# Performance work log

Measured on AMD Instinct MI355X. Metric: run time of the kernel, lower is better.

The kernel has to match this reference:

```python
import jax, jax.numpy as jnp
import numpy as np

N = 50000      # n_nodes
E = 800000     # n_edges (avg degree 16)
IN, HID, CLS = 128, 128, 40


def setup_inputs() -> dict:
    key = jax.random.key(0)
    ks = jax.random.split(key, 9)
    features = jax.random.normal(ks[0], (N, IN), dtype=jnp.float32)
    src = jax.random.randint(ks[1], (E,), 0, N)
    dst = jax.random.randint(ks[2], (E,), 0, N)
    # GraphConv weights (glorot-ish scale) and biases
    W0 = jax.random.normal(ks[3], (IN, HID), dtype=jnp.float32) / np.sqrt(IN).astype(np.float32)
    b0 = jnp.zeros((HID,), jnp.float32)
    W1 = jax.random.normal(ks[4], (HID, HID), dtype=jnp.float32) / np.sqrt(HID).astype(np.float32)
    b1 = jnp.zeros((HID,), jnp.float32)
    W2 = jax.random.normal(ks[5], (HID, CLS), dtype=jnp.float32) / np.sqrt(HID).astype(np.float32)
    b2 = jnp.zeros((CLS,), jnp.float32)
    return {"features": features, "src": src, "dst": dst,
            "W0": W0, "b0": b0, "W1": W1, "b1": b1, "W2": W2, "b2": b2}


def _degree_norms(src, dst, dtype):
    # DGL GraphConv norm='both': D_out^{-1/2} on source side, D_in^{-1/2} on dest side,
    # degrees clamped to a minimum of 1.
    ones = jnp.ones(src.shape[0], dtype)
    deg_out = jax.ops.segment_sum(ones, src, num_segments=N)
    deg_in = jax.ops.segment_sum(ones, dst, num_segments=N)
    norm_out = jnp.where(deg_out > 0, deg_out, 1.0) ** -0.5
    norm_in = jnp.where(deg_in > 0, deg_in, 1.0) ** -0.5
    return norm_out, norm_in


def _graph_conv(h, src, dst, norm_out, norm_in, W, b, act):
    # h' = D_in^{-1/2} A D_out^{-1/2} h W + b ; optional relu
    h = (h * norm_out[:, None]) @ W            # dense transform first (in >= out)
    agg = jax.ops.segment_sum(h[src], dst, num_segments=N)  # sparse aggregation
    out = agg * norm_in[:, None] + b
    return jax.nn.relu(out) if act else out


def reference(features, src, dst, W0, b0, W1, b1, W2, b2):
    norm_out, norm_in = _degree_norms(src, dst, features.dtype)
    # dropout is identity in eval mode
    h = _graph_conv(features, src, dst, norm_out, norm_in, W0, b0, True)
    h = _graph_conv(h, src, dst, norm_out, norm_in, W1, b1, True)
    h = _graph_conv(h, src, dst, norm_out, norm_in, W2, b2, False)
    return h
```

## Files before the change

kernel.cpp:

```cpp
#include <hip/hip_runtime.h>
#include <hip/hip_fp16.h>


static constexpr int NN  = 50000;
static constexpr int NE  = 800000;
static constexpr int HID = 128;
static constexpr int CLS = 40;
static constexpr int CAP = 48;

static constexpr int NGEMM  = (NN + 127) / 128;
static constexpr int NBUILD = (NE + 1023) / 1024;
static constexpr int NPREP  = 8;

typedef __attribute__((ext_vector_type(8))) _Float16 f16x8;
typedef __attribute__((ext_vector_type(4))) float    f32x4;

__device__ __forceinline__ void gemm128_body(const float* __restrict__ X,
                                             const float* __restrict__ W,
                                             __half* __restrict__ Y,
                                             int tileIdx, float* As, float* Bs) {
    constexpr int BSTR = 132;
    const int tid = threadIdx.x;
    const int rowBase = tileIdx * 128;

    const int bkk = tid >> 3;
    const int bc4 = tid & 7;
    const float* wrow = W + (size_t)bkk * 128 + bc4 * 16;

    const int rt = tid & 15;
    const int ct = tid >> 4;

    float acc[8][8];
    #pragma unroll
    for (int j = 0; j < 8; ++j)
        #pragma unroll
        for (int i = 0; i < 8; ++i) acc[j][i] = 0.f;

    float4 xv[4], wv[4];

    auto loadA = [&](int s) {
        #pragma unroll
        for (int i = 0; i < 4; ++i) {
            int f = tid + 256 * i;
            int r = f >> 3;
            int kc = f & 7;
            int grow = rowBase + r;
            xv[i] = (grow < NN)
                ? *(const float4*)(X + (size_t)grow * 128 + s * 32 + kc * 4)
                : make_float4(0.f, 0.f, 0.f, 0.f);
        }
    };
    auto loadB = [&](int s) {
        const float* p = wrow + (size_t)s * 32 * 128;
        #pragma unroll
        for (int i = 0; i < 4; ++i) wv[i] = ((const float4*)p)[i];
    };
    auto writeLDS = [&]() {
        #pragma unroll
        for (int i = 0; i < 4; ++i) {
            int f = tid + 256 * i;
            int r = f >> 3;
            int kc = f & 7;
            int pc = ((r >> 2) + kc) & 31;
            int base = pc * 4 + (r & 3);
            const float* v = (const float*)&xv[i];
            #pragma unroll
            for (int c = 0; c < 4; ++c)
                As[(kc * 4 + c) * 128 + base] = v[c];
        }
        #pragma unroll
        for (int i = 0; i < 4; ++i)
            *(float4*)&Bs[bkk * BSTR + bc4 * 16 + i * 4] = wv[i];
    };

    loadA(0); loadB(0);
    for (int s = 0; s < 4; ++s) {
        writeLDS();
        __syncthreads();
        if (s < 3) { loadA(s + 1); loadB(s + 1); }
        #pragma unroll 8
        for (int k = 0; k < 32; ++k) {
            int kc = k >> 2;
            int pa0 = (rt + kc) & 31;
            int pa1 = (rt + 16 + kc) & 31;
            float4 a0 = *(const float4*)&As[k * 128 + pa0 * 4];
            float4 a1 = *(const float4*)&As[k * 128 + pa1 * 4];
            float4 b0 = *(const float4*)&Bs[k * BSTR + ct * 8];
            float4 b1 = *(const float4*)&Bs[k * BSTR + ct * 8 + 4];
            float a[8] = {a0.x, a0.y, a0.z, a0.w, a1.x, a1.y, a1.z, a1.w};
            float b[8] = {b0.x, b0.y, b0.z, b0.w, b1.x, b1.y, b1.z, b1.w};
            #pragma unroll
            for (int j = 0; j < 8; ++j)
                #pragma unroll
                for (int ii = 0; ii < 8; ++ii)
                    acc[j][ii] = fmaf(a[j], b[ii], acc[j][ii]);
        }
        __syncthreads();
    }
    union Pack { __half2 h2[4]; uint4 u; };
    #pragma unroll
    for (int j = 0; j < 8; ++j) {
        int row = rowBase + ((j < 4) ? (4 * rt + j) : (64 + 4 * rt + (j - 4)));
        if (row < NN) {
            Pack p;
            #pragma unroll
            for (int q = 0; q < 4; ++q)
                p.h2[q] = __halves2half2(__float2half_rn(acc[j][2 * q]),
                                         __float2half_rn(acc[j][2 * q + 1]));
            *(uint4*)(Y + (size_t)row * 128 + ct * 8) = p.u;
        }
    }
}

__global__ __launch_bounds__(256) void fused_kernel(const float* __restrict__ X,
                                                    const float* __restrict__ W0,
                                                    __half* __restrict__ Y,
                                                    const int* __restrict__ src,
                                                    const int* __restrict__ dst,
                                                    int* __restrict__ deg_out,
                                                    int* __restrict__ cnt,
                                                    unsigned short* __restrict__ colbkt,
                                                    const float* __restrict__ W1,
                                                    __half* __restrict__ W1t) {
    __shared__ float As[32 * 128];
    __shared__ float Bs[32 * 132];
    int b = blockIdx.x;
    if (b < NGEMM) {
        gemm128_body(X, W0, Y, b, As, Bs);
    } else if (b < NGEMM + NBUILD) {
        int base = (b - NGEMM) * 1024 + threadIdx.x;
        int e[4], s[4], d[4];
        #pragma unroll
        for (int i = 0; i < 4; ++i) {
            e[i] = base + 256 * i;
            int ec = e[i] < NE ? e[i] : NE - 1;
            s[i] = src[ec];
            d[i] = dst[ec];
        }
        #pragma unroll
        for (int i = 0; i < 4; ++i)
            if (e[i] < NE) atomicAdd(&deg_out[s[i]], 1);
        int slot[4];
        #pragma unroll
        for (int i = 0; i < 4; ++i)
            slot[i] = (e[i] < NE) ? atomicAdd(&cnt[d[i]], 1) : CAP;
        #pragma unroll
        for (int i = 0; i < 4; ++i)
            if (slot[i] < CAP)
                colbkt[(size_t)d[i] * CAP + slot[i]] = (unsigned short)s[i];
    } else {
        int gid = (b - NGEMM - NBUILD) * 256 + threadIdx.x;
        int n = gid >> 4, q = gid & 15;
        union { __half h[8]; uint4 u; } p;
        #pragma unroll
        for (int j = 0; j < 8; ++j)
            p.h[j] = __float2half_rn(W1[(size_t)(q * 8 + j) * 128 + n]);
        ((uint4*)W1t)[n * 16 + ((q + n) & 15)] = p.u;
    }
}

__global__ __launch_bounds__(256) void gemm1_mfma(const __half* __restrict__ H,
                                                  const __half* __restrict__ W1t,
                                                  const float* __restrict__ norm_out,
                                                  __half* __restrict__ T) {
    __shared__ __half Ws[128 * 128];
    const int tid = threadIdx.x;
    #pragma unroll
    for (int i = 0; i < 8; ++i)
        ((uint4*)Ws)[tid + 256 * i] = ((const uint4*)W1t)[tid + 256 * i];

    const int wv   = tid >> 6;
    const int lane = tid & 63;
    const int m    = lane & 15;
    const int quad = lane >> 4;
    const int rowW = blockIdx.x * 64 + wv * 16;

    union AB { uint4 u; f16x8 h; };
    AB a[4];
    int arow = rowW + m;
    if (arow >= NN) arow = NN - 1;
    const uint4* hp = (const uint4*)(H + (size_t)arow * 128);
    #pragma unroll
    for (int kc = 0; kc < 4; ++kc)
        a[kc].u = hp[kc * 4 + quad];

    __syncthreads();

    f32x4 acc[8];
    #pragma unroll
    for (int nt = 0; nt < 8; ++nt) acc[nt] = (f32x4){0.f, 0.f, 0.f, 0.f};

    #pragma unroll
    for (int kc = 0; kc < 4; ++kc) {
        #pragma unroll
        for (int nt = 0; nt < 8; ++nt) {
            int n = nt * 16 + m;
            int q = kc * 4 + quad;
            AB bf;
            bf.u = ((const uint4*)Ws)[n * 16 + ((q + n) & 15)];
            acc[nt] = __builtin_amdgcn_mfma_f32_16x16x32_f16(a[kc].h, bf.h, acc[nt], 0, 0, 0);
        }
    }

    float nmv[4];
    #pragma unroll
    for (int r = 0; r < 4; ++r) {
        int row = rowW + quad * 4 + r;
        nmv[r] = (row < NN) ? norm_out[row] : 0.f;
    }
    #pragma unroll
    for (int nt = 0; nt < 8; ++nt) {
        int coln = nt * 16 + m;
        #pragma unroll
        for (int r = 0; r < 4; ++r) {
            int row = rowW + quad * 4 + r;
            if (row < NN)
                T[(size_t)row * 128 + coln] = __float2half_rn(acc[nt][r] * nmv[r]);
        }
    }
}

__global__ __launch_bounds__(256) void gemm40_kernel(const __half* __restrict__ X,
                                                     const float* __restrict__ W,
                                                     const float* __restrict__ norm_out,
                                                     __half* __restrict__ Y) {
    __shared__ float As[32 * 128];
    __shared__ float Bs[32 * 40];
    const int tid = threadIdx.x;
    const int rowBase = blockIdx.x * 128;

    const int rt = tid & 31;
    const int ct = tid >> 5;

    float acc[4][5];
    #pragma unroll
    for (int j = 0; j < 4; ++j)
        #pragma unroll
        for (int c = 0; c < 5; ++c) acc[j][c] = 0.f;

    uint4 xu[2];
    float4 wv[2];

    auto loadA = [&](int s) {
        #pragma unroll
        for (int i = 0; i < 2; ++i) {
            int f = tid + 256 * i;
            int r = f >> 2;
            int c = f & 3;
            int grow = rowBase + r;
            xu[i] = (grow < NN)
                ? *(const uint4*)(X + (size_t)grow * 128 + s * 32 + c * 8)
                : make_uint4(0, 0, 0, 0);
        }
    };
    auto loadB = [&](int s) {
        #pragma unroll
        for (int i = 0; i < 2; ++i) {
            int f = tid + 256 * i;
            if (f < 320) {
                int kk = f / 10, c4 = f - kk * 10;
                wv[i] = *(const float4*)(W + (size_t)(s * 32 + kk) * 40 + c4 * 4);
            }
        }
    };
    auto writeLDS = [&]() {
        #pragma unroll
        for (int i = 0; i < 2; ++i) {
            int f = tid + 256 * i;
            int r = f >> 2;
            int c = f & 3;
            const __half2* hp = (const __half2*)&xu[i];
            #pragma unroll
            for (int q = 0; q < 4; ++q) {
                float2 f2 = __half22float2(hp[q]);
                int k0 = c * 8 + 2 * q;
                int pc = ((r >> 2) + (k0 >> 2)) & 31;
                As[k0 * 128 + pc * 4 + (r & 3)]       = f2.x;
                As[(k0 + 1) * 128 + pc * 4 + (r & 3)] = f2.y;
            }
        }
        #pragma unroll
        for (int i = 0; i < 2; ++i) {
            int f = tid + 256 * i;
            if (f < 320) {
                int kk = f / 10, c4 = f - kk * 10;
                *(float4*)&Bs[kk * 40 + c4 * 4] = wv[i];
            }
        }
    };

    loadA(0); loadB(0);
    for (int s = 0; s < 4; ++s) {
        writeLDS();
        __syncthreads();
        if (s < 3) { loadA(s + 1); loadB(s + 1); }
        #pragma unroll 8
        for (int k = 0; k < 32; ++k) {
            int kc = k >> 2;
            int pa = (rt + kc) & 31;
            float4 av4 = *(const float4*)&As[k * 128 + pa * 4];
            float av[4] = {av4.x, av4.y, av4.z, av4.w};
            float bv[5];
            #pragma unroll
            for (int c = 0; c < 5; ++c) bv[c] = Bs[k * 40 + ct * 5 + c];
            #pragma unroll
            for (int j = 0; j < 4; ++j)
                #pragma unroll
                for (int c = 0; c < 5; ++c)
                    acc[j][c] = fmaf(av[j], bv[c], acc[j][c]);
        }
        __syncthreads();
    }
    #pragma unroll
    for (int j = 0; j < 4; ++j) {
        int row = rowBase + rt * 4 + j;
        if (row < NN) {
            float nm = norm_out[row];
            #pragma unroll
            for (int c = 0; c < 5; ++c)
                Y[(size_t)row * 40 + ct * 5 + c] = __float2half_rn(acc[j][c] * nm);
        }
    }
}

__global__ __launch_bounds__(256) void norm_scale_kernel(const int* __restrict__ deg_out,
                                                         const int* __restrict__ cnt,
                                                         float* __restrict__ norm_out,
                                                         float* __restrict__ norm_in,
                                                         __half* __restrict__ t) {
    __shared__ float nms[32];
    int base = blockIdx.x * 32;
    int tid = threadIdx.x;
    if (tid < 32) {
        int v = base + tid;
        float no = 1.f;
        if (v < NN) {
            int dof = deg_out[v], dif = cnt[v];
            no = rsqrtf((float)(dof > 0 ? dof : 1));
            norm_out[v] = no;
            norm_in[v]  = rsqrtf((float)(dif > 0 ? dif : 1));
        }
        nms[tid] = no;
    }
    __syncthreads();
    for (int i = tid; i < 512; i += 256) {
        int ro = i >> 4, ch = i & 15;
        int v = base + ro;
        if (v < NN) {
            uint4* p = (uint4*)t + (size_t)v * 16 + ch;
            uint4 u = *p;
            float nm = nms[ro];
            __half2* hp = (__half2*)&u;
            #pragma unroll
            for (int q = 0; q < 4; ++q) {
                float2 f = __half22float2(hp[q]);
                hp[q] = __halves2half2(__float2half_rn(f.x * nm),
                                       __float2half_rn(f.y * nm));
            }
            *p = u;
        }
    }
}

__global__ __launch_bounds__(256) void agg128h_kernel(const __half* __restrict__ T,
                                                      const unsigned short* __restrict__ colbkt,
                                                      const int* __restrict__ cnt,
                                                      const float* __restrict__ norm_in,
                                                      const float* __restrict__ bias,
                                                      __half* __restrict__ out) {
    int node = blockIdx.x * 4 + (threadIdx.x >> 6);
    int lane = threadIdx.x & 63;
    if (node >= NN) return;
    int dg = cnt[node];
    if (dg > CAP) dg = CAP;
    const unsigned short* bkt = colbkt + (size_t)node * CAP;
    const int grp = lane >> 4;
    const int l16 = lane & 15;

    float acc[8];
    #pragma unroll
    for (int i = 0; i < 8; ++i) acc[i] = 0.f;

    constexpr int B = 4;
    for (int j = 0; j < dg; j += 4 * B) {
        uint4 v[B];
        float w[B];
        #pragma unroll
        for (int u = 0; u < B; ++u) {
            int e  = j + 4 * u + grp;
            int ec = e < dg ? e : dg - 1;
            int s  = (int)bkt[ec];
            w[u]   = e < dg ? 1.f : 0.f;
            v[u]   = ((const uint4*)(T + (size_t)s * 128))[l16];
        }
        #pragma unroll
        for (int u = 0; u < B; ++u) {
            const __half2* hp = (const __half2*)&v[u];
            #pragma unroll
            for (int q = 0; q < 4; ++q) {
                float2 f = __half22float2(hp[q]);
                acc[2 * q]     = fmaf(f.x, w[u], acc[2 * q]);
                acc[2 * q + 1] = fmaf(f.y, w[u], acc[2 * q + 1]);
            }
        }
    }
    #pragma unroll
    for (int i = 0; i < 8; ++i) {
        acc[i] += __shfl_xor(acc[i], 16, 64);
        acc[i] += __shfl_xor(acc[i], 32, 64);
    }
    if (grp == 0) {
        float nm = norm_in[node];
        float4 b0 = ((const float4*)bias)[l16 * 2];
        float4 b1 = ((const float4*)bias)[l16 * 2 + 1];
        float o[8];
        o[0] = fmaf(acc[0], nm, b0.x); o[1] = fmaf(acc[1], nm, b0.y);
        o[2] = fmaf(acc[2], nm, b0.z); o[3] = fmaf(acc[3], nm, b0.w);
        o[4] = fmaf(acc[4], nm, b1.x); o[5] = fmaf(acc[5], nm, b1.y);
        o[6] = fmaf(acc[6], nm, b1.z); o[7] = fmaf(acc[7], nm, b1.w);
        union { __half2 h2[4]; uint4 u; } pk;
        #pragma unroll
        for (int q = 0; q < 4; ++q) {
            float x = fmaxf(o[2 * q], 0.f);
            float y = fmaxf(o[2 * q + 1], 0.f);
            pk.h2[q] = __halves2half2(__float2half_rn(x), __float2half_rn(y));
        }
        ((uint4*)(out + (size_t)node * 128))[l16] = pk.u;
    }
}

__global__ __launch_bounds__(256) void agg40h_kernel(const __half* __restrict__ T,
                                                     const unsigned short* __restrict__ colbkt,
                                                     const int* __restrict__ cnt,
                                                     const float* __restrict__ norm_in,
                                                     const float* __restrict__ bias,
                                                     float* __restrict__ out) {
    int node = blockIdx.x * 4 + (threadIdx.x >> 6);
    int lane = threadIdx.x & 63;
    if (node >= NN) return;
    int dg = cnt[node];
    if (dg > CAP) dg = CAP;
    const unsigned short* bkt = colbkt + (size_t)node * CAP;
    const int grp = lane / 20;
    const int l20 = lane - grp * 20;

    float accx = 0.f, accy = 0.f;
    constexpr int B = 4;
    for (int j = 0; j < dg; j += 3 * B) {
        unsigned int v[B];
        float w[B];
        #pragma unroll
        for (int u = 0; u < B; ++u) {
            int e  = j + 3 * u + grp;
            bool p = (grp < 3) && (e < dg);
            int ec = e < dg ? e : dg - 1;
            int s  = (grp < 3) ? (int)bkt[ec] : 0;
            w[u]   = p ? 1.f : 0.f;
            v[u]   = *(const unsigned int*)(T + (size_t)s * 40 + l20 * 2);
        }
        #pragma unroll
        for (int u = 0; u < B; ++u) {
            float2 f = __half22float2(*(const __half2*)&v[u]);
            accx = fmaf(f.x, w[u], accx);
            accy = fmaf(f.y, w[u], accy);
        }
    }
    accx += __shfl(accx, lane + 20, 64) + __shfl(accx, lane + 40, 64);
    accy += __shfl(accy, lane + 20, 64) + __shfl(accy, lane + 40, 64);

    if (lane < 20) {
        float nm = norm_in[node];
        float2 b = *(const float2*)(bias + lane * 2);
        float ox = fmaf(accx, nm, b.x);
        float oy = fmaf(accy, nm, b.y);
        *(float2*)(out + (size_t)node * 40 + lane * 2) = make_float2(ox, oy);
    }
}

extern "C" void kernel_launch(void* const* d_in, const int* in_sizes, int n_in,
                              void* d_out, int out_size, void* d_ws, size_t ws_size,
                              hipStream_t stream) {
    const float* features = (const float*)d_in[0];
    const int*   src      = (const int*)d_in[1];
    const int*   dst      = (const int*)d_in[2];
    const float* W0       = (const float*)d_in[3];
    const float* b0       = (const float*)d_in[4];
    const float* W1       = (const float*)d_in[5];
    const float* b1       = (const float*)d_in[6];
    const float* W2       = (const float*)d_in[7];
    const float* b2       = (const float*)d_in[8];
    float*       out      = (float*)d_out;

    char* ws = (char*)d_ws;
    auto alloc = [&](size_t bytes) {
        char* p = ws;
        ws += (bytes + 511) & ~(size_t)511;
        return p;
    };
    int*            deg_out  = (int*)alloc((size_t)NN * 4);
    int*            cnt      = (int*)alloc((size_t)NN * 4);
    float*          norm_out = (float*)alloc((size_t)NN * 4);
    float*          norm_in  = (float*)alloc((size_t)NN * 4);
    unsigned short* colbkt   = (unsigned short*)alloc((size_t)NN * CAP * 2);
    __half*         W1t      = (__half*)alloc((size_t)HID * HID * 2);
    __half*         t        = (__half*)alloc((size_t)NN * HID * 2);
    __half*         h        = (__half*)alloc((size_t)NN * HID * 2);
    if ((size_t)(ws - (char*)d_ws) > ws_size) return;

    hipMemsetAsync(deg_out, 0, (size_t)NN * 4, stream);
    hipMemsetAsync(cnt, 0, (size_t)NN * 4, stream);

    int gAgg = (NN + 3) / 4;

    fused_kernel<<<NGEMM + NBUILD + NPREP, 256, 0, stream>>>(
        features, W0, t, src, dst, deg_out, cnt, colbkt, W1, W1t);
    norm_scale_kernel<<<(NN + 31) / 32, 256, 0, stream>>>(deg_out, cnt, norm_out, norm_in, t);

    agg128h_kernel<<<gAgg, 256, 0, stream>>>(t, colbkt, cnt, norm_in, b0, h);
    gemm1_mfma<<<(NN + 63) / 64, 256, 0, stream>>>(h, W1t, norm_out, t);
    agg128h_kernel<<<gAgg, 256, 0, stream>>>(t, colbkt, cnt, norm_in, b1, h);
    gemm40_kernel<<<NGEMM, 256, 0, stream>>>(h, W2, norm_out, t);
    agg40h_kernel<<<(NN + 3) / 4, 256, 0, stream>>>(t, colbkt, cnt, norm_in, b2, out);
}
```

Baseline: 288.1 us.

## Use MFMA for the 40-class GEMM with padded 48-wide fp16 layout

```diff
diff --git a/kernel.cpp b/kernel.cpp
--- a/kernel.cpp
+++ b/kernel.cpp
@@ -10,10 +10,12 @@
 
 static constexpr int NGEMM  = (NN + 127) / 128;
 static constexpr int NBUILD = (NE + 1023) / 1024;
-static constexpr int NPREP  = 8;
+static constexpr int NPREP1 = 8;
+static constexpr int NPREP2 = 3;
 
 typedef __attribute__((ext_vector_type(8))) _Float16 f16x8;
 typedef __attribute__((ext_vector_type(4))) float    f32x4;
+union ABu { uint4 u; f16x8 h; };
 
 __device__ __forceinline__ void gemm128_body(const float* __restrict__ X,
                                              const float* __restrict__ W,
@@ -121,7 +123,9 @@
                                                     int* __restrict__ cnt,
                                                     unsigned short* __restrict__ colbkt,
                                                     const float* __restrict__ W1,
-                                                    __half* __restrict__ W1t) {
+                                                    __half* __restrict__ W1t,
+                                                    const float* __restrict__ W2,
+                                                    __half* __restrict__ W2t) {
     __shared__ float As[32 * 128];
     __shared__ float Bs[32 * 132];
     int b = blockIdx.x;
@@ -148,7 +152,7 @@
         for (int i = 0; i < 4; ++i)
             if (slot[i] < CAP)
                 colbkt[(size_t)d[i] * CAP + slot[i]] = (unsigned short)s[i];
-    } else {
+    } else if (b < NGEMM + NBUILD + NPREP1) {
         int gid = (b - NGEMM - NBUILD) * 256 + threadIdx.x;
         int n = gid >> 4, q = gid & 15;
         union { __half h[8]; uint4 u; } p;
@@ -156,6 +160,71 @@
         for (int j = 0; j < 8; ++j)
             p.h[j] = __float2half_rn(W1[(size_t)(q * 8 + j) * 128 + n]);
         ((uint4*)W1t)[n * 16 + ((q + n) & 15)] = p.u;
+    } else {
+        int gid = (b - NGEMM - NBUILD - NPREP1) * 256 + threadIdx.x;
+        int n = gid >> 4, q = gid & 15;
+        union { __half h[8]; uint4 u; } p;
+        #pragma unroll
+        for (int j = 0; j < 8; ++j)
+            p.h[j] = (n < CLS) ? __float2half_rn(W2[(size_t)(q * 8 + j) * CLS + n])
+                               : __half(0.f);
+        ((uint4*)W2t)[n * 16 + ((q + n) & 15)] = p.u;
+    }
+}
+
+template <int NT>
+__device__ __forceinline__ void mfma_rowgemm_body(const __half* __restrict__ H,
+                                                  const float* __restrict__ norm_out,
+                                                  __half* __restrict__ Y,
+                                                  const __half* Ws) {
+    const int tid  = threadIdx.x;
+    const int wv   = tid >> 6;
+    const int lane = tid & 63;
+    const int m    = lane & 15;
+    const int quad = lane >> 4;
+    const int rowW = blockIdx.x * 64 + wv * 16;
+
+    ABu a[4];
+    int arow = rowW + m;
+    if (arow >= NN) arow = NN - 1;
+    const uint4* hp = (const uint4*)(H + (size_t)arow * 128);
+    #pragma unroll
+    for (int kc = 0; kc < 4; ++kc)
+        a[kc].u = hp[kc * 4 + quad];
+
+    __syncthreads();
+
+    f32x4 acc[NT];
+    #pragma unroll
+    for (int nt = 0; nt < NT; ++nt) acc[nt] = (f32x4){0.f, 0.f, 0.f, 0.f};
+
+    #pragma unroll
+    for (int kc = 0; kc < 4; ++kc) {
+        #pragma unroll
+        for (int nt = 0; nt < NT; ++nt) {
+            int n = nt * 16 + m;
+            int q = kc * 4 + quad;
+            ABu bf;
+            bf.u = ((const uint4*)Ws)[n * 16 + ((q + n) & 15)];
+            acc[nt] = __builtin_amdgcn_mfma_f32_16x16x32_f16(a[kc].h, bf.h, acc[nt], 0, 0, 0);
+        }
+    }
+
+    float nmv[4];
+    #pragma unroll
+    for (int r = 0; r < 4; ++r) {
+        int row = rowW + quad * 4 + r;
+        nmv[r] = (row < NN) ? norm_out[row] : 0.f;
+    }
+    #pragma unroll
+    for (int nt = 0; nt < NT; ++nt) {
+        int coln = nt * 16 + m;
+        #pragma unroll
+        for (int r = 0; r < 4; ++r) {
+            int row = rowW + quad * 4 + r;
+            if (row < NN)
+                Y[(size_t)row * (NT * 16) + coln] = __float2half_rn(acc[nt][r] * nmv[r]);
+        }
     }
 }
 
@@ -168,159 +237,19 @@
     #pragma unroll
     for (int i = 0; i < 8; ++i)
         ((uint4*)Ws)[tid + 256 * i] = ((const uint4*)W1t)[tid + 256 * i];
-
-    const int wv   = tid >> 6;
-    const int lane = tid & 63;
-    const int m    = lane & 15;
-    const int quad = lane >> 4;
-    const int rowW = blockIdx.x * 64 + wv * 16;
-
-    union AB { uint4 u; f16x8 h; };
-    AB a[4];
-    int arow = rowW + m;
-    if (arow >= NN) arow = NN - 1;
-    const uint4* hp = (const uint4*)(H + (size_t)arow * 128);
-    #pragma unroll
-    for (int kc = 0; kc < 4; ++kc)
-        a[kc].u = hp[kc * 4 + quad];
-
-    __syncthreads();
-
-    f32x4 acc[8];
-    #pragma unroll
-    for (int nt = 0; nt < 8; ++nt) acc[nt] = (f32x4){0.f, 0.f, 0.f, 0.f};
-
-    #pragma unroll
-    for (int kc = 0; kc < 4; ++kc) {
-        #pragma unroll
-        for (int nt = 0; nt < 8; ++nt) {
-            int n = nt * 16 + m;
-            int q = kc * 4 + quad;
-            AB bf;
-            bf.u = ((const uint4*)Ws)[n * 16 + ((q + n) & 15)];
-            acc[nt] = __builtin_amdgcn_mfma_f32_16x16x32_f16(a[kc].h, bf.h, acc[nt], 0, 0, 0);
-        }
-    }
-
-    float nmv[4];
-    #pragma unroll
-    for (int r = 0; r < 4; ++r) {
-        int row = rowW + quad * 4 + r;
-        nmv[r] = (row < NN) ? norm_out[row] : 0.f;
-    }
-    #pragma unroll
-    for (int nt = 0; nt < 8; ++nt) {
-        int coln = nt * 16 + m;
-        #pragma unroll
-        for (int r = 0; r < 4; ++r) {
-            int row = rowW + quad * 4 + r;
-            if (row < NN)
-                T[(size_t)row * 128 + coln] = __float2half_rn(acc[nt][r] * nmv[r]);
-        }
-    }
-}
-
-__global__ __launch_bounds__(256) void gemm40_kernel(const __half* __restrict__ X,
-                                                     const float* __restrict__ W,
-                                                     const float* __restrict__ norm_out,
-                                                     __half* __restrict__ Y) {
-    __shared__ float As[32 * 128];
-    __shared__ float Bs[32 * 40];
+    mfma_rowgemm_body<8>(H, norm_out, T, Ws);
+}
+
+__global__ __launch_bounds__(256) void gemm40_mfma(const __half* __restrict__ H,
+                                                   const __half* __restrict__ W2t,
+                                                   const float* __restrict__ norm_out,
+                                                   __half* __restrict__ T40) {
+    __shared__ __half Ws[48 * 128];
     const int tid = threadIdx.x;
-    const int rowBase = blockIdx.x * 128;
-
-    const int rt = tid & 31;
-    const int ct = tid >> 5;
-
-    float acc[4][5];
-    #pragma unroll
-    for (int j = 0; j < 4; ++j)
-        #pragma unroll
-        for (int c = 0; c < 5; ++c) acc[j][c] = 0.f;
-
-    uint4 xu[2];
-    float4 wv[2];
-
-    auto loadA = [&](int s) {
-        #pragma unroll
-        for (int i = 0; i < 2; ++i) {
-            int f = tid + 256 * i;
-            int r = f >> 2;
-            int c = f & 3;
-            int grow = rowBase + r;
-            xu[i] = (grow < NN)
-                ? *(const uint4*)(X + (size_t)grow * 128 + s * 32 + c * 8)
-                : make_uint4(0, 0, 0, 0);
-        }
-    };
-    auto loadB = [&](int s) {
-        #pragma unroll
-        for (int i = 0; i < 2; ++i) {
-            int f = tid + 256 * i;
-            if (f < 320) {
-                int kk = f / 10, c4 = f - kk * 10;
-                wv[i] = *(const float4*)(W + (size_t)(s * 32 + kk) * 40 + c4 * 4);
-            }
-        }
-    };
-    auto writeLDS = [&]() {
-        #pragma unroll
-        for (int i = 0; i < 2; ++i) {
-            int f = tid + 256 * i;
-            int r = f >> 2;
-            int c = f & 3;
-            const __half2* hp = (const __half2*)&xu[i];
-            #pragma unroll
-            for (int q = 0; q < 4; ++q) {
-                float2 f2 = __half22float2(hp[q]);
-                int k0 = c * 8 + 2 * q;
-                int pc = ((r >> 2) + (k0 >> 2)) & 31;
-                As[k0 * 128 + pc * 4 + (r & 3)]       = f2.x;
-                As[(k0 + 1) * 128 + pc * 4 + (r & 3)] = f2.y;
-            }
-        }
-        #pragma unroll
-        for (int i = 0; i < 2; ++i) {
-            int f = tid + 256 * i;
-            if (f < 320) {
-                int kk = f / 10, c4 = f - kk * 10;
-                *(float4*)&Bs[kk * 40 + c4 * 4] = wv[i];
-            }
-        }
-    };
-
-    loadA(0); loadB(0);
-    for (int s = 0; s < 4; ++s) {
-        writeLDS();
-        __syncthreads();
-        if (s < 3) { loadA(s + 1); loadB(s + 1); }
-        #pragma unroll 8
-        for (int k = 0; k < 32; ++k) {
-            int kc = k >> 2;
-            int pa = (rt + kc) & 31;
-            float4 av4 = *(const float4*)&As[k * 128 + pa * 4];
-            float av[4] = {av4.x, av4.y, av4.z, av4.w};
-            float bv[5];
-            #pragma unroll
-            for (int c = 0; c < 5; ++c) bv[c] = Bs[k * 40 + ct * 5 + c];
-            #pragma unroll
-            for (int j = 0; j < 4; ++j)
-                #pragma unroll
-                for (int c = 0; c < 5; ++c)
-                    acc[j][c] = fmaf(av[j], bv[c], acc[j][c]);
-        }
-        __syncthreads();
-    }
-    #pragma unroll
-    for (int j = 0; j < 4; ++j) {
-        int row = rowBase + rt * 4 + j;
-        if (row < NN) {
-            float nm = norm_out[row];
-            #pragma unroll
-            for (int c = 0; c < 5; ++c)
-                Y[(size_t)row * 40 + ct * 5 + c] = __float2half_rn(acc[j][c] * nm);
-        }
-    }
+    #pragma unroll
+    for (int i = 0; i < 3; ++i)
+        ((uint4*)Ws)[tid + 256 * i] = ((const uint4*)W2t)[tid + 256 * i];
+    mfma_rowgemm_body<3>(H, norm_out, T40, Ws);
 }
 
 __global__ __launch_bounds__(256) void norm_scale_kernel(const int* __restrict__ deg_out,
@@ -441,39 +370,57 @@
     int dg = cnt[node];
     if (dg > CAP) dg = CAP;
     const unsigned short* bkt = colbkt + (size_t)node * CAP;
-    const int grp = lane / 20;
-    const int l20 = lane - grp * 20;
-
-    float accx = 0.f, accy = 0.f;
+    const int g = lane / 6;
+    const int c = lane - g * 6;
+
+    float acc[8];
+    #pragma unroll
+    for (int i = 0; i < 8; ++i) acc[i] = 0.f;
+
     constexpr int B = 4;
-    for (int j = 0; j < dg; j += 3 * B) {
-        unsigned int v[B];
+    for (int j = 0; j < dg; j += 8 * B) {
+        uint4 v[B];
         float w[B];
         #pragma unroll
         for (int u = 0; u < B; ++u) {
-            int e  = j + 3 * u + grp;
-            bool p = (grp < 3) && (e < dg);
-            int ec = e < dg ? e : dg - 1;
-            int s  = (grp < 3) ? (int)bkt[ec] : 0;
+            int e  = j + 8 * u + g;
+            bool p = (g < 8) && (e < dg);
+            int ec = p ? e : 0;
+            int s  = (int)bkt[ec];
             w[u]   = p ? 1.f : 0.f;
-            v[u]   = *(const unsigned int*)(T + (size_t)s * 40 + l20 * 2);
+            v[u]   = ((const uint4*)(T + (size_t)s * 48))[c];
         }
         #pragma unroll
         for (int u = 0; u < B; ++u) {
-            float2 f = __half22float2(*(const __half2*)&v[u]);
-            accx = fmaf(f.x, w[u], accx);
-            accy = fmaf(f.y, w[u], accy);
-        }
-    }
-    accx += __shfl(accx, lane + 20, 64) + __shfl(accx, lane + 40, 64);
-    accy += __shfl(accy, lane + 20, 64) + __shfl(accy, lane + 40, 64);
-
-    if (lane < 20) {
+            const __half2* hp = (const __half2*)&v[u];
+            #pragma unroll
+            for (int q = 0; q < 4; ++q) {
+                float2 f = __half22float2(hp[q]);
+                acc[2 * q]     = fmaf(f.x, w[u], acc[2 * q]);
+                acc[2 * q + 1] = fmaf(f.y, w[u], acc[2 * q + 1]);
+            }
+        }
+    }
+    #pragma unroll
+    for (int i = 0; i < 8; ++i) {
+        acc[i] += __shfl(acc[i], lane + 24, 64);
+        acc[i] += __shfl(acc[i], lane + 12, 64);
+        acc[i] += __shfl(acc[i], lane + 6, 64);
+    }
+    if (lane < 5) {
         float nm = norm_in[node];
-        float2 b = *(const float2*)(bias + lane * 2);
-        float ox = fmaf(accx, nm, b.x);
-        float oy = fmaf(accy, nm, b.y);
-        *(float2*)(out + (size_t)node * 40 + lane * 2) = make_float2(ox, oy);
+        float4 o0, o1;
+        o0.x = fmaf(acc[0], nm, bias[c * 8 + 0]);
+        o0.y = fmaf(acc[1], nm, bias[c * 8 + 1]);
+        o0.z = fmaf(acc[2], nm, bias[c * 8 + 2]);
+        o0.w = fmaf(acc[3], nm, bias[c * 8 + 3]);
+        o1.x = fmaf(acc[4], nm, bias[c * 8 + 4]);
+        o1.y = fmaf(acc[5], nm, bias[c * 8 + 5]);
+        o1.z = fmaf(acc[6], nm, bias[c * 8 + 6]);
+        o1.w = fmaf(acc[7], nm, bias[c * 8 + 7]);
+        float* op = out + (size_t)node * 40 + c * 8;
+        *(float4*)op       = o0;
+        *(float4*)(op + 4) = o1;
     }
 }
 
@@ -503,22 +450,25 @@
     float*          norm_in  = (float*)alloc((size_t)NN * 4);
     unsigned short* colbkt   = (unsigned short*)alloc((size_t)NN * CAP * 2);
     __half*         W1t      = (__half*)alloc((size_t)HID * HID * 2);
+    __half*         W2t      = (__half*)alloc((size_t)48 * HID * 2);
     __half*         t        = (__half*)alloc((size_t)NN * HID * 2);
     __half*         h        = (__half*)alloc((size_t)NN * HID * 2);
+    __half*         t40      = (__half*)alloc((size_t)NN * 48 * 2);
     if ((size_t)(ws - (char*)d_ws) > ws_size) return;
 
     hipMemsetAsync(deg_out, 0, (size_t)NN * 4, stream);
     hipMemsetAsync(cnt, 0, (size_t)NN * 4, stream);
 
     int gAgg = (NN + 3) / 4;
-
-    fused_kernel<<<NGEMM + NBUILD + NPREP, 256, 0, stream>>>(
-        features, W0, t, src, dst, deg_out, cnt, colbkt, W1, W1t);
+    int gRow64 = (NN + 63) / 64;
+
+    fused_kernel<<<NGEMM + NBUILD + NPREP1 + NPREP2, 256, 0, stream>>>(
+        features, W0, t, src, dst, deg_out, cnt, colbkt, W1, W1t, W2, W2t);
     norm_scale_kernel<<<(NN + 31) / 32, 256, 0, stream>>>(deg_out, cnt, norm_out, norm_in, t);
 
     agg128h_kernel<<<gAgg, 256, 0, stream>>>(t, colbkt, cnt, norm_in, b0, h);
-    gemm1_mfma<<<(NN + 63) / 64, 256, 0, stream>>>(h, W1t, norm_out, t);
+    gemm1_mfma<<<gRow64, 256, 0, stream>>>(h, W1t, norm_out, t);
     agg128h_kernel<<<gAgg, 256, 0, stream>>>(t, colbkt, cnt, norm_in, b1, h);
-    gemm40_kernel<<<NGEMM, 256, 0, stream>>>(h, W2, norm_out, t);
-    agg40h_kernel<<<(NN + 3) / 4, 256, 0, stream>>>(t, colbkt, cnt, norm_in, b2, out);
-}
+    gemm40_mfma<<<gRow64, 256, 0, stream>>>(h, W2t, norm_out, t40);
+    agg40h_kernel<<<gAgg, 256, 0, stream>>>(t40, colbkt, cnt, norm_in, b2, out);
+}
```

Result: faster. 263.5 us (-8.5%).
